# Kernel tuning notes

Hardware: AMD Instinct MI355X
Metric: run time of the kernel (lower is better)

The kernel has to match this reference:

```python
import jax, jax.numpy as jnp
import numpy as np


def setup_inputs() -> dict:
    key = jax.random.key(0)
    ks = jax.random.split(key, 9)
    bs, F, T, d_in, Nh, d_out = 4, 8, 256, 64, 8, 64
    std = 2.0  # gaussian_init_delta_std
    return {
        "X": jax.random.normal(ks[0], (bs, F, T, d_in), dtype=jnp.float32),
        "attention_center": std * jax.random.normal(ks[1], (F, Nh, 1), dtype=jnp.float32),
        "alpha": jax.random.normal(ks[2], (F,), dtype=jnp.float32),
        "W_query": jax.random.normal(ks[3], (F, T, d_in, Nh, 2), dtype=jnp.float32),
        "W_key": jax.random.normal(ks[4], (F, T, d_in, Nh, 2), dtype=jnp.float32),
        "Wkey_": jax.random.normal(ks[5], (F, 2, 2), dtype=jnp.float32),
        "u": jax.random.normal(ks[6], (F, T, 2), dtype=jnp.float32),
        "W": jax.random.normal(ks[7], (F, Nh * d_in, d_out), dtype=jnp.float32),
        "b": jax.random.normal(ks[8], (F, T, d_out), dtype=jnp.float32),
    }


def reference(X, attention_center, alpha, W_query, W_key, Wkey_, u, W, b):
    bs, F, T, d_in = X.shape
    Nh = W_query.shape[3]

    # relative-position features R[t,l] = (l-t)^2, (l-t); identical across F in the original
    rel = (jnp.arange(T)[None, :] - jnp.arange(T)[:, None]).astype(jnp.float32)
    R = jnp.stack([rel ** 2, rel], axis=-1)  # (T,T,2)

    query = jnp.einsum('bftd,ftdhe->bfthe', X, W_query)  # (bs,F,T,Nh,2)
    key = jnp.einsum('bftd,ftdhe->bfthe', X, W_key)      # (bs,F,T,Nh,2)

    r_delta = jnp.einsum('fde,tle->ftld', Wkey_, R)      # (F,T,T,2)

    centers = jnp.concatenate([jnp.ones_like(attention_center), -2.0 * attention_center], axis=-1)  # (F,Nh,2)
    v = -alpha[:, None, None] * centers                  # (F,Nh,2)

    scores = (
        jnp.einsum('bfthe,bflhe->bfthl', query, key)
        + jnp.einsum('bfthe,ftle->bfthl', query, r_delta)
        + jnp.einsum('fle,bfthe->bfthl', u, key)
        + jnp.einsum('fhe,ftle->fthl', v, r_delta)[None]
    )  # (bs,F,T,Nh,T)

    probs = jax.nn.softmax(scores, axis=-1)

    vals = jnp.einsum('bfthl,bfld->bfthd', probs, X)     # (bs,F,T,Nh,d_in)
    vals = vals.reshape(bs, F, T, Nh * d_in)

    return jnp.einsum('bftd,fdo->bfto', vals, W) + b     # (bs,F,T,d_out)
```

## Files before the change

### kernel.cpp

```cpp
#include <hip/hip_runtime.h>
#include <hip/hip_bf16.h>

#define BS 4
#define NF 8
#define NT 256
#define DIN 64
#define NH 8
#define DOUT 64
#define TT 4
#define MROWS 32
#define NCH 64

typedef unsigned short u16;
typedef __attribute__((ext_vector_type(8))) short short8;
typedef __attribute__((ext_vector_type(4))) float f32x4;
typedef __attribute__((ext_vector_type(4))) unsigned int u32x4;

static __device__ __forceinline__ u16 f2bf(float x) {
    __hip_bfloat16 h = __float2bfloat16(x);
    u16 r; __builtin_memcpy(&r, &h, 2); return r;
}
static __device__ __forceinline__ unsigned pk2(float a, float b) {
    return (unsigned)f2bf(a) | ((unsigned)f2bf(b) << 16);
}

__global__ __launch_bounds__(256) void prep_kernel(
    const float* __restrict__ X,
    const float* __restrict__ Wq,
    const float* __restrict__ Wk,
    const float* __restrict__ W,
    float* __restrict__ q,
    float* __restrict__ k,
    u16* __restrict__ XT,
    u16* __restrict__ Wt)
{
    __shared__ float sT[64][65];
    __shared__ float sXq[4 * 256];
    const int tid = threadIdx.x;
    const int bid = blockIdx.x;

    if (bid < 1024) {
        const int wv = tid >> 6, L = tid & 63;
        const int gw = (bid << 2) + wv;
        const int which = gw >> 11;
        const int ft = gw & 2047;
        const int f = ft >> 8, t = ft & 255;

        const float* wmat = which ? Wk : Wq;
        const float* wp = wmat + ((size_t)ft << 10);
        float4 w0 = *(const float4*)(wp + (L << 2));
        float4 w1 = *(const float4*)(wp + 256 + (L << 2));
        float4 w2 = *(const float4*)(wp + 512 + (L << 2));
        float4 w3 = *(const float4*)(wp + 768 + (L << 2));

        float* sx = sXq + (wv << 8);
        {
            int xb = L >> 4, d4 = (L & 15) << 2;
            *(float4*)(sx + (xb << 6) + d4) =
                *(const float4*)(X + (((size_t)((xb * NF + f) * NT + t)) << 6) + d4);
        }
        const int dr = L >> 2;
        float4 acc[4];
        #pragma unroll
        for (int bb = 0; bb < 4; ++bb) {
            float x0 = sx[(bb << 6) + dr];
            float x1 = sx[(bb << 6) + 16 + dr];
            float x2 = sx[(bb << 6) + 32 + dr];
            float x3 = sx[(bb << 6) + 48 + dr];
            float4 a;
            a.x = fmaf(x0, w0.x, fmaf(x1, w1.x, fmaf(x2, w2.x, x3 * w3.x)));
            a.y = fmaf(x0, w0.y, fmaf(x1, w1.y, fmaf(x2, w2.y, x3 * w3.y)));
            a.z = fmaf(x0, w0.z, fmaf(x1, w1.z, fmaf(x2, w2.z, x3 * w3.z)));
            a.w = fmaf(x0, w0.w, fmaf(x1, w1.w, fmaf(x2, w2.w, x3 * w3.w)));
            acc[bb] = a;
        }
        #pragma unroll
        for (int off = 4; off <= 32; off <<= 1) {
            #pragma unroll
            for (int bb = 0; bb < 4; ++bb) {
                acc[bb].x += __shfl_xor(acc[bb].x, off);
                acc[bb].y += __shfl_xor(acc[bb].y, off);
                acc[bb].z += __shfl_xor(acc[bb].z, off);
                acc[bb].w += __shfl_xor(acc[bb].w, off);
            }
        }
        if (L < 4) {
            float* outp = which ? k : q;
            #pragma unroll
            for (int bb = 0; bb < 4; ++bb)
                *(float4*)(outp + (((size_t)((bb * NF + f) * NT + t)) << 4) + (L << 2)) = acc[bb];
        }
    } else if (bid < 1056) {
        const int bf = bid - 1024;
        for (int lc = 0; lc < 4; ++lc) {
            #pragma unroll
            for (int i = 0; i < 16; ++i) {
                int l = i * 4 + (tid >> 6), d = tid & 63;
                sT[l][d] = X[(((size_t)(bf * NT) + lc * 64 + l) << 6) + d];
            }
            __syncthreads();
            #pragma unroll
            for (int i = 0; i < 16; ++i) {
                int d = i * 4 + (tid >> 6), l = tid & 63;
                XT[(((size_t)(bf * 64) + d) << 8) + lc * 64 + l] = f2bf(sT[l][d]);
            }
            __syncthreads();
        }
    } else {
        const int idx = bid - 1056;
        const int f = idx >> 3, kc = idx & 7;
        #pragma unroll
        for (int i = 0; i < 16; ++i) {
            int kk = i * 4 + (tid >> 6), o = tid & 63;
            sT[kk][o] = W[(((size_t)(f * 512) + kc * 64 + kk) << 6) + o];
        }
        __syncthreads();
        #pragma unroll
        for (int i = 0; i < 16; ++i) {
            int o = i * 4 + (tid >> 6), kk = tid & 63;
            Wt[(((size_t)(f * 64) + o) << 9) + kc * 64 + kk] = f2bf(sT[kk][o]);
        }
    }
}

__global__ __launch_bounds__(256, 4) void attn_kernel(
    const float* __restrict__ ac,
    const float* __restrict__ alpha,
    const float* __restrict__ Wkey_,
    const float* __restrict__ u,
    const float* __restrict__ bias,
    const float* __restrict__ q,
    const float* __restrict__ kws,
    const u16* __restrict__ XT,
    const u16* __restrict__ Wt,
    float* __restrict__ out)
{
    __shared__ u16  sP[MROWS * 256];
    __shared__ float sKU[4608];
    __shared__ float sRed[MROWS * 16];
    __shared__ float sM[MROWS];
    __shared__ float sInvS[MROWS];

    const int tid = threadIdx.x;
    const int bid = blockIdx.x;
    const int ch = bid & 63;
    const int f  = (bid >> 6) & 7;
    const int b  = bid >> 9;
    const int bf = b * NF + f;
    const int t0 = ch * TT;

    {
        const float4* k4 = (const float4*)(kws + ((size_t)bf << 12));
        float4* d4 = (float4*)sKU;
        #pragma unroll
        for (int i = 0; i < 4; ++i) d4[i * 256 + tid] = k4[i * 256 + tid];
        if (tid < 128) ((float4*)(sKU + 4096))[tid] = ((const float4*)(u + f * 512))[tid];
    }
    __syncthreads();

    const int h  = tid & 7;
    const int tp = (tid >> 3) & 1;
    const int lg = tid >> 4;
    const int t_a = t0 + tp * 2, t_b = t_a + 1;
    const int m_a = tp * 16 + h, m_b = m_a + 8;
    const int lbase = lg * 16;

    float q0a, q1a, kt0a, kt1a, c2a, c1a;
    float q0b, q1b, kt0b, kt1b, c2b, c1b;
    {
        float al = alpha[f];
        float acv = ac[f * 8 + h];
        float wk0 = Wkey_[f * 4],     wk1 = Wkey_[f * 4 + 1];
        float wk2 = Wkey_[f * 4 + 2], wk3 = Wkey_[f * 4 + 3];
        float2 qa = *(const float2*)(q + ((size_t)(bf * NT + t_a) << 4) + (h << 1));
        float2 qb = *(const float2*)(q + ((size_t)(bf * NT + t_b) << 4) + (h << 1));
        q0a = qa.x; q1a = qa.y; q0b = qb.x; q1b = qb.y;
        kt0a = sKU[t_a * 16 + h * 2]; kt1a = sKU[t_a * 16 + h * 2 + 1];
        kt0b = sKU[t_b * 16 + h * 2]; kt1b = sKU[t_b * 16 + h * 2 + 1];
        float a0 = q0a - al, a1 = q1a + 2.f * al * acv;
        c2a = a0 * wk0 + a1 * wk2; c1a = a0 * wk1 + a1 * wk3;
        a0 = q0b - al; a1 = q1b + 2.f * al * acv;
        c2b = a0 * wk0 + a1 * wk2; c1b = a0 * wk1 + a1 * wk3;
    }

    float sA[16], sB[16];
    float mxa = -1e30f, mxb = -1e30f;
    {
        float rela = (float)(lbase - t_a);
        #pragma unroll
        for (int j = 0; j < 16; ++j) {
            int l = lbase + j;
            float2 K = *(const float2*)(sKU + l * 16 + h * 2);
            float2 U = *(const float2*)(sKU + 4096 + l * 2);
            float relb = rela - 1.f;
            float sa = (c2a * rela + c1a) * rela;
            sa = fmaf(q0a, K.x, sa); sa = fmaf(q1a, K.y, sa);
            sa = fmaf(kt0a, U.x, sa); sa = fmaf(kt1a, U.y, sa);
            float sb = (c2b * relb + c1b) * relb;
            sb = fmaf(q0b, K.x, sb); sb = fmaf(q1b, K.y, sb);
            sb = fmaf(kt0b, U.x, sb); sb = fmaf(kt1b, U.y, sb);
            sA[j] = sa; sB[j] = sb;
            mxa = fmaxf(mxa, sa); mxb = fmaxf(mxb, sb);
            rela += 1.f;
        }
    }
    sRed[m_a * 16 + lg] = mxa;
    sRed[m_b * 16 + lg] = mxb;
    __syncthreads();
    if (tid < MROWS) {
        const float4* r4 = (const float4*)(sRed + tid * 16);
        float4 r0 = r4[0], r1 = r4[1], r2 = r4[2], r3 = r4[3];
        float mm = fmaxf(fmaxf(fmaxf(r0.x, r0.y), fmaxf(r0.z, r0.w)),
                         fmaxf(fmaxf(r1.x, r1.y), fmaxf(r1.z, r1.w)));
        mm = fmaxf(mm, fmaxf(fmaxf(fmaxf(r2.x, r2.y), fmaxf(r2.z, r2.w)),
                             fmaxf(fmaxf(r3.x, r3.y), fmaxf(r3.z, r3.w))));
        sM[tid] = mm;
    }
    __syncthreads();

    {
        const float Ma = sM[m_a], Mb = sM[m_b];
        float suma = 0.f, sumb = 0.f;
        unsigned pka[4], pkb[4];
        float epa = 0.f, epb = 0.f;
        #pragma unroll
        for (int j = 0; j < 16; ++j) {
            float ea = __expf(sA[j] - Ma), eb = __expf(sB[j] - Mb);
            suma += ea; sumb += eb;
            if ((j & 1) == 0) { epa = ea; epb = eb; }
            else { pka[(j & 7) >> 1] = pk2(epa, ea); pkb[(j & 7) >> 1] = pk2(epb, eb); }
            if ((j & 7) == 7) {
                int chunk = lg * 2 + (j >> 3);
                int pa = chunk ^ h;
                int pb = chunk ^ (h + 8);
                *(u32x4*)&sP[m_a * 256 + pa * 8] = (u32x4){pka[0], pka[1], pka[2], pka[3]};
                *(u32x4*)&sP[m_b * 256 + pb * 8] = (u32x4){pkb[0], pkb[1], pkb[2], pkb[3]};
            }
        }
        sRed[m_a * 16 + lg] = suma;
        sRed[m_b * 16 + lg] = sumb;
    }

    const int wv   = tid >> 6;
    const int lane = tid & 63;
    const int quad = lane >> 4;
    const int ln   = lane & 15;
    const int mh   = wv & 1;
    const int nh   = wv >> 1;
    const u16* xb = XT + ((size_t)bf << 14);
    short8 nb0, nb1;
    {
        int l2 = quad * 8;
        nb0 = *(const short8*)(xb + (nh * 32 + ln) * 256 + l2);
        nb1 = *(const short8*)(xb + (nh * 32 + 16 + ln) * 256 + l2);
    }
    __syncthreads();
    if (tid < MROWS) {
        const float4* r4 = (const float4*)(sRed + tid * 16);
        float4 r0 = r4[0], r1 = r4[1], r2 = r4[2], r3 = r4[3];
        float ss = ((r0.x + r0.y) + (r0.z + r0.w)) + ((r1.x + r1.y) + (r1.z + r1.w))
                 + ((r2.x + r2.y) + (r2.z + r2.w)) + ((r3.x + r3.y) + (r3.z + r3.w));
        sInvS[tid] = 1.f / ss;
    }
    __syncthreads();

    f32x4 acc0 = {0.f, 0.f, 0.f, 0.f}, acc1 = acc0;
    #pragma unroll
    for (int ks = 0; ks < 8; ++ks) {
        short8 b0 = nb0, b1 = nb1;
        if (ks < 7) {
            int l2 = (ks + 1) * 32 + quad * 8;
            nb0 = *(const short8*)(xb + (nh * 32 + ln) * 256 + l2);
            nb1 = *(const short8*)(xb + (nh * 32 + 16 + ln) * 256 + l2);
        }
        int phys = (ks * 4 + quad) ^ ln;
        short8 a = *(const short8*)&sP[(mh * 16 + ln) * 256 + phys * 8];
        acc0 = __builtin_amdgcn_mfma_f32_16x16x32_bf16(a, b0, acc0, 0, 0, 0);
        acc1 = __builtin_amdgcn_mfma_f32_16x16x32_bf16(a, b1, acc1, 0, 0, 0);
    }

    u16* sVals = (u16*)sKU;
    #pragma unroll
    for (int reg = 0; reg < 4; ++reg) {
        int mg = mh * 16 + quad * 4 + reg;
        float inv = sInvS[mg];
        int tl = mg >> 3, hh = mg & 7;
        u16* dst = sVals + tl * 520 + hh * 64 + nh * 32 + ln;
        dst[0]  = f2bf(acc0[reg] * inv);
        dst[16] = f2bf(acc1[reg] * inv);
    }
    const u16* wb = Wt + ((size_t)(f * 64 + wv * 16 + ln) << 9);
    short8 nw = *(const short8*)(wb + quad * 8);
    __syncthreads();

    f32x4 oacc = {0.f, 0.f, 0.f, 0.f};
    #pragma unroll
    for (int ks = 0; ks < 16; ++ks) {
        short8 bw = nw;
        if (ks < 15) nw = *(const short8*)(wb + (ks + 1) * 32 + quad * 8);
        short8 a = *(const short8*)(sVals + ln * 520 + ks * 32 + quad * 8);
        oacc = __builtin_amdgcn_mfma_f32_16x16x32_bf16(a, bw, oacc, 0, 0, 0);
    }
    {
        int o = wv * 16 + ln;
        #pragma unroll
        for (int reg = 0; reg < 4; ++reg) {
            int tl = quad * 4 + reg;
            if (tl < TT) {
                int tg = t0 + tl;
                out[((size_t)(bf * NT + tg) << 6) + o] =
                    oacc[reg] + bias[((size_t)(f * NT + tg) << 6) + o];
            }
        }
    }
}

extern "C" void kernel_launch(void* const* d_in, const int* in_sizes, int n_in,
                              void* d_out, int out_size, void* d_ws, size_t ws_size,
                              hipStream_t stream) {
    const float* X     = (const float*)d_in[0];
    const float* ac    = (const float*)d_in[1];
    const float* alpha = (const float*)d_in[2];
    const float* Wq    = (const float*)d_in[3];
    const float* Wk    = (const float*)d_in[4];
    const float* Wkey_ = (const float*)d_in[5];
    const float* u     = (const float*)d_in[6];
    const float* W     = (const float*)d_in[7];
    const float* bb    = (const float*)d_in[8];
    float* out = (float*)d_out;

    float* qws = (float*)d_ws;
    float* kws = qws + 131072;
    u16* XT = (u16*)(kws + 131072);
    u16* Wt = XT + 524288;

    hipLaunchKernelGGL(prep_kernel, dim3(1120), dim3(256), 0, stream,
                       X, Wq, Wk, W, qws, kws, XT, Wt);
    hipLaunchKernelGGL(attn_kernel, dim3(BS * NF * NCH), dim3(256), 0, stream,
                       ac, alpha, Wkey_, u, bb, qws, kws, XT, Wt, out);
}
```

Baseline: 119.0 us.

## Restructure prep kernel Q/K projection via shared-memory transpose and split X transpose blocks

The Q/K projection now gives one block per (f,t), handling both Wq and Wk. Weights are staged transposed into padded shared memory, and each pair of threads computes one output element with a two-lane shuffle reduction, replacing the per-wave multi-stage shuffle tree. The X-to-bf16 transpose is also split from 32 blocks, each looping over 4 chunks, into 128 blocks of one chunk each. This raises parallelism in the prep stage and shortens the long-running transpose blocks, at the cost of a block-wide barrier and more blocks launched.

Result: no change. 118.4 us (-0.5%).

```diff
diff --git a/kernel.cpp b/kernel.cpp
--- a/kernel.cpp
+++ b/kernel.cpp
@@ -34,81 +34,73 @@
     u16* __restrict__ XT,
     u16* __restrict__ Wt)
 {
-    __shared__ float sT[64][65];
-    __shared__ float sXq[4 * 256];
+    __shared__ float sm[4160];
     const int tid = threadIdx.x;
     const int bid = blockIdx.x;
 
-    if (bid < 1024) {
-        const int wv = tid >> 6, L = tid & 63;
-        const int gw = (bid << 2) + wv;
-        const int which = gw >> 11;
-        const int ft = gw & 2047;
+    if (bid < 2048) {
+        const int ft = bid;
         const int f = ft >> 8, t = ft & 255;
-
-        const float* wmat = which ? Wk : Wq;
-        const float* wp = wmat + ((size_t)ft << 10);
-        float4 w0 = *(const float4*)(wp + (L << 2));
-        float4 w1 = *(const float4*)(wp + 256 + (L << 2));
-        float4 w2 = *(const float4*)(wp + 512 + (L << 2));
-        float4 w3 = *(const float4*)(wp + 768 + (L << 2));
-
-        float* sx = sXq + (wv << 8);
+        float* sWt = sm;
+        float* sX  = sm + 2176;
+
+        float4 a4 = ((const float4*)(Wq + ((size_t)ft << 10)))[tid];
+        float4 b4 = ((const float4*)(Wk + ((size_t)ft << 10)))[tid];
         {
-            int xb = L >> 4, d4 = (L & 15) << 2;
-            *(float4*)(sx + (xb << 6) + d4) =
-                *(const float4*)(X + (((size_t)((xb * NF + f) * NT + t)) << 6) + d4);
-        }
-        const int dr = L >> 2;
-        float4 acc[4];
-        #pragma unroll
-        for (int bb = 0; bb < 4; ++bb) {
-            float x0 = sx[(bb << 6) + dr];
-            float x1 = sx[(bb << 6) + 16 + dr];
-            float x2 = sx[(bb << 6) + 32 + dr];
-            float x3 = sx[(bb << 6) + 48 + dr];
-            float4 a;
-            a.x = fmaf(x0, w0.x, fmaf(x1, w1.x, fmaf(x2, w2.x, x3 * w3.x)));
-            a.y = fmaf(x0, w0.y, fmaf(x1, w1.y, fmaf(x2, w2.y, x3 * w3.y)));
-            a.z = fmaf(x0, w0.z, fmaf(x1, w1.z, fmaf(x2, w2.z, x3 * w3.z)));
-            a.w = fmaf(x0, w0.w, fmaf(x1, w1.w, fmaf(x2, w2.w, x3 * w3.w)));
-            acc[bb] = a;
-        }
-        #pragma unroll
-        for (int off = 4; off <= 32; off <<= 1) {
-            #pragma unroll
-            for (int bb = 0; bb < 4; ++bb) {
-                acc[bb].x += __shfl_xor(acc[bb].x, off);
-                acc[bb].y += __shfl_xor(acc[bb].y, off);
-                acc[bb].z += __shfl_xor(acc[bb].z, off);
-                acc[bb].w += __shfl_xor(acc[bb].w, off);
-            }
-        }
-        if (L < 4) {
+            int d = tid >> 2, he = (tid & 3) << 2;
+            sWt[(he + 0) * 68 + d] = a4.x;
+            sWt[(he + 1) * 68 + d] = a4.y;
+            sWt[(he + 2) * 68 + d] = a4.z;
+            sWt[(he + 3) * 68 + d] = a4.w;
+            sWt[1088 + (he + 0) * 68 + d] = b4.x;
+            sWt[1088 + (he + 1) * 68 + d] = b4.y;
+            sWt[1088 + (he + 2) * 68 + d] = b4.z;
+            sWt[1088 + (he + 3) * 68 + d] = b4.w;
+            int xb = tid >> 6, xd = tid & 63;
+            sX[tid] = X[(((size_t)((xb * NF + f) * NT + t)) << 6) + xd];
+        }
+        __syncthreads();
+
+        const int half  = tid & 1;
+        const int he    = (tid >> 1) & 15;
+        const int b     = (tid >> 5) & 3;
+        const int which = tid >> 7;
+        const float* wp = sWt + which * 1088 + he * 68 + (half << 5);
+        const float* xp = sX + (b << 6) + (half << 5);
+        float acc = 0.f;
+        #pragma unroll
+        for (int j = 0; j < 8; ++j) {
+            float4 w = *(const float4*)(wp + (j << 2));
+            float4 x = *(const float4*)(xp + (j << 2));
+            acc = fmaf(w.x, x.x, acc);
+            acc = fmaf(w.y, x.y, acc);
+            acc = fmaf(w.z, x.z, acc);
+            acc = fmaf(w.w, x.w, acc);
+        }
+        acc += __shfl_xor(acc, 1);
+        if (half == 0) {
             float* outp = which ? k : q;
-            #pragma unroll
-            for (int bb = 0; bb < 4; ++bb)
-                *(float4*)(outp + (((size_t)((bb * NF + f) * NT + t)) << 4) + (L << 2)) = acc[bb];
-        }
-    } else if (bid < 1056) {
-        const int bf = bid - 1024;
-        for (int lc = 0; lc < 4; ++lc) {
-            #pragma unroll
-            for (int i = 0; i < 16; ++i) {
-                int l = i * 4 + (tid >> 6), d = tid & 63;
-                sT[l][d] = X[(((size_t)(bf * NT) + lc * 64 + l) << 6) + d];
-            }
-            __syncthreads();
-            #pragma unroll
-            for (int i = 0; i < 16; ++i) {
-                int d = i * 4 + (tid >> 6), l = tid & 63;
-                XT[(((size_t)(bf * 64) + d) << 8) + lc * 64 + l] = f2bf(sT[l][d]);
-            }
-            __syncthreads();
+            outp[(((size_t)((b * NF + f) * NT + t)) << 4) + he] = acc;
+        }
+    } else if (bid < 2176) {
+        const int idx = bid - 2048;
+        const int bf = idx >> 2, lc = idx & 3;
+        float (*sT)[65] = (float(*)[65])sm;
+        #pragma unroll
+        for (int i = 0; i < 16; ++i) {
+            int l = i * 4 + (tid >> 6), d = tid & 63;
+            sT[l][d] = X[(((size_t)(bf * NT) + lc * 64 + l) << 6) + d];
+        }
+        __syncthreads();
+        #pragma unroll
+        for (int i = 0; i < 16; ++i) {
+            int d = i * 4 + (tid >> 6), l = tid & 63;
+            XT[(((size_t)(bf * 64) + d) << 8) + lc * 64 + l] = f2bf(sT[l][d]);
         }
     } else {
-        const int idx = bid - 1056;
+        const int idx = bid - 2176;
         const int f = idx >> 3, kc = idx & 7;
+        float (*sT)[65] = (float(*)[65])sm;
         #pragma unroll
         for (int i = 0; i < 16; ++i) {
             int kk = i * 4 + (tid >> 6), o = tid & 63;
@@ -334,7 +326,7 @@
     u16* XT = (u16*)(kws + 131072);
     u16* Wt = XT + 524288;
 
-    hipLaunchKernelGGL(prep_kernel, dim3(1120), dim3(256), 0, stream,
+    hipLaunchKernelGGL(prep_kernel, dim3(2240), dim3(256), 0, stream,
                        X, Wq, Wk, W, qws, kws, XT, Wt);
     hipLaunchKernelGGL(attn_kernel, dim3(BS * NF * NCH), dim3(256), 0, stream,
                        ac, alpha, Wkey_, u, bb, qws, kws, XT, Wt, out);
```
